# Kernel optimization log

Measured on AMD Instinct MI355X. Metric: run time of the kernel, lower is better.

Reference implementation:

```python
import jax, jax.numpy as jnp
import numpy as np

N_NODES = 100000
IN_DIM = 512
OUT_DIM = 16
N_EDGES = 3200000


def setup_inputs() -> dict:
    key = jax.random.key(0)
    k1, k2, k3, k4 = jax.random.split(key, 4)
    x = jax.random.normal(k1, (N_NODES, IN_DIM), dtype=jnp.float32)
    edge_index = jax.random.randint(k2, (2, N_EDGES), 0, N_NODES, dtype=jnp.int64)
    # GCNConv params (glorot weight, zero bias as in PyG)
    scale = jnp.sqrt(6.0 / (IN_DIM + OUT_DIM)).astype(jnp.float32)
    W = jax.random.uniform(k3, (IN_DIM, OUT_DIM), dtype=jnp.float32, minval=-scale, maxval=scale)
    b = jnp.zeros((OUT_DIM,), dtype=jnp.float32)
    return {"x": x, "edge_index": edge_index, "W": W, "b": b}


def reference(x, edge_index, W, b):
    n = x.shape[0]
    # GCNConv with normalize=True: add self-loops, symmetric deg normalization
    loops = jnp.arange(n, dtype=edge_index.dtype)
    row = jnp.concatenate([edge_index[0], loops])  # source nodes
    col = jnp.concatenate([edge_index[1], loops])  # target nodes

    h = x @ W  # [N, 16] dense linear transform

    deg = jax.ops.segment_sum(jnp.ones_like(col, dtype=h.dtype), col, num_segments=n)
    dinv = jnp.where(deg > 0, jax.lax.rsqrt(jnp.maximum(deg, 1.0)), 0.0)
    norm = dinv[row] * dinv[col]  # [E+N]

    # gather source features, scale, scatter-add into targets
    out = jax.ops.segment_sum(norm[:, None] * h[row], col, num_segments=n)
    return out + b
```

## Files before the change

kernel.cpp:

```cpp
#include <hip/hip_runtime.h>
#include <hip/hip_fp16.h>

#define IN_DIM 512
#define OUT_DIM 16
#define KC 32
#define TILE_ROWS 256

#define BSHIFT 8
#define BNODES 256
#define MAXBUCK 512
#define BCOUNT_CHUNK 4096
#define BIN_CHUNK 4096

__global__ __launch_bounds__(256) void gemm_wave(const float* __restrict__ x,
                                                 const float* __restrict__ W,
                                                 const int* __restrict__ hist,
                                                 __half* __restrict__ hp, int n) {
    __shared__ float xs[4 * 64 * (KC + 1)];
    const int tid = threadIdx.x;
    const int lane = tid & 63;
    const int wid = __builtin_amdgcn_readfirstlane(tid >> 6);
    const int rbase = blockIdx.x * 256 + wid * 64;
    if (rbase >= n) return;
    const int myrow = rbase + lane;

    float* xw = xs + wid * (64 * (KC + 1));
    const int srow = lane >> 3;
    const int scol = (lane & 7) << 2;

    float4 stA[8], stB[8];

#define LOADC(buf, c)                                                          \
    {                                                                          \
        _Pragma("unroll")                                                      \
        for (int i = 0; i < 8; ++i) {                                          \
            const int rr = rbase + 8 * i + srow;                               \
            if (rr < n)                                                        \
                buf[i] = *(const float4*)(x + (size_t)rr * IN_DIM + (c) * KC + scol); \
            else                                                               \
                buf[i] = make_float4(0.f, 0.f, 0.f, 0.f);                      \
        }                                                                      \
    }

#define STOREC(buf)                                                            \
    {                                                                          \
        _Pragma("unroll")                                                      \
        for (int i = 0; i < 8; ++i) {                                          \
            float* d = xw + (8 * i + srow) * (KC + 1) + scol;                  \
            d[0] = buf[i].x; d[1] = buf[i].y; d[2] = buf[i].z; d[3] = buf[i].w; \
        }                                                                      \
    }

#define COMPUTEC(c)                                                            \
    {                                                                          \
        const float* xrow = xw + lane * (KC + 1);                              \
        const float* Wb = W + (size_t)(c) * KC * OUT_DIM;                      \
        _Pragma("unroll 4")                                                    \
        for (int k = 0; k < KC; ++k) {                                         \
            const float xv = xrow[k];                                          \
            const float* wr = Wb + k * OUT_DIM;                                \
            const float4 w0 = *(const float4*)(wr + 0);                        \
            const float4 w1 = *(const float4*)(wr + 4);                        \
            const float4 w2 = *(const float4*)(wr + 8);                        \
            const float4 w3 = *(const float4*)(wr + 12);                       \
            acc[0]  += xv * w0.x; acc[1]  += xv * w0.y; acc[2]  += xv * w0.z; acc[3]  += xv * w0.w; \
            acc[4]  += xv * w1.x; acc[5]  += xv * w1.y; acc[6]  += xv * w1.z; acc[7]  += xv * w1.w; \
            acc[8]  += xv * w2.x; acc[9]  += xv * w2.y; acc[10] += xv * w2.z; acc[11] += xv * w2.w; \
            acc[12] += xv * w3.x; acc[13] += xv * w3.y; acc[14] += xv * w3.z; acc[15] += xv * w3.w; \
        }                                                                      \
    }

    float acc[OUT_DIM];
#pragma unroll
    for (int j = 0; j < OUT_DIM; ++j) acc[j] = 0.f;

    LOADC(stA, 0);
    for (int cc = 0; cc < 8; ++cc) {
        const int c0 = 2 * cc, c1 = 2 * cc + 1;
        STOREC(stA);
        LOADC(stB, c1);
        COMPUTEC(c0);
        STOREC(stB);
        if (c1 + 1 < 16) LOADC(stA, c1 + 1);
        COMPUTEC(c1);
    }

    if (myrow < n) {
        const float s = rsqrtf((float)(hist[myrow] + 1));
        __half2* op = (__half2*)(hp + (size_t)myrow * OUT_DIM);
#pragma unroll
        for (int j = 0; j < 8; ++j)
            op[j] = __floats2half2_rn(s * acc[2 * j], s * acc[2 * j + 1]);
    }
#undef LOADC
#undef STOREC
#undef COMPUTEC
}

__global__ __launch_bounds__(256) void gemm_xw(const float* __restrict__ x,
                                               const float* __restrict__ W,
                                               const int* __restrict__ hist,
                                               __half* __restrict__ hp, int n) {
    __shared__ float xs[TILE_ROWS * (KC + 1)];
    const int tid = threadIdx.x;
    const int rbase = blockIdx.x * TILE_ROWS;
    const int myrow = rbase + tid;

    float acc[OUT_DIM];
#pragma unroll
    for (int j = 0; j < OUT_DIM; ++j) acc[j] = 0.f;

    for (int kc = 0; kc < IN_DIM; kc += KC) {
        __syncthreads();
#pragma unroll
        for (int i = 0; i < 8; ++i) {
            const int v = tid + 256 * i;
            const int r = v >> 3;
            const int c = (v & 7) << 2;
            if (rbase + r < n) {
                const float4 f = *(const float4*)(x + (size_t)(rbase + r) * IN_DIM + kc + c);
                float* d = xs + r * (KC + 1) + c;
                d[0] = f.x; d[1] = f.y; d[2] = f.z; d[3] = f.w;
            }
        }
        __syncthreads();

        const float* xrow = xs + tid * (KC + 1);
#pragma unroll 4
        for (int k = 0; k < KC; ++k) {
            const float xv = xrow[k];
            const float* wr = W + (size_t)(kc + k) * OUT_DIM;
            const float4 w0 = *(const float4*)(wr + 0);
            const float4 w1 = *(const float4*)(wr + 4);
            const float4 w2 = *(const float4*)(wr + 8);
            const float4 w3 = *(const float4*)(wr + 12);
            acc[0]  += xv * w0.x; acc[1]  += xv * w0.y; acc[2]  += xv * w0.z; acc[3]  += xv * w0.w;
            acc[4]  += xv * w1.x; acc[5]  += xv * w1.y; acc[6]  += xv * w1.z; acc[7]  += xv * w1.w;
            acc[8]  += xv * w2.x; acc[9]  += xv * w2.y; acc[10] += xv * w2.z; acc[11] += xv * w2.w;
            acc[12] += xv * w3.x; acc[13] += xv * w3.y; acc[14] += xv * w3.z; acc[15] += xv * w3.w;
        }
    }

    if (myrow < n) {
        const float s = rsqrtf((float)(hist[myrow] + 1));
        __half2* op = (__half2*)(hp + (size_t)myrow * OUT_DIM);
#pragma unroll
        for (int j = 0; j < 8; ++j)
            op[j] = __floats2half2_rn(s * acc[2 * j], s * acc[2 * j + 1]);
    }
}

__device__ inline void scan512_excl(const int* src, int* dst, int lane) {
    int c[8], pre[8];
    int tot = 0;
#pragma unroll
    for (int k = 0; k < 8; ++k) { c[k] = src[lane * 8 + k]; pre[k] = tot; tot += c[k]; }
    int incl = tot;
#pragma unroll
    for (int d = 1; d < 64; d <<= 1) {
        const int u = __shfl_up(incl, d);
        if (lane >= d) incl += u;
    }
    const int excl = incl - tot;
#pragma unroll
    for (int k = 0; k < 8; ++k) dst[lane * 8 + k] = excl + pre[k];
}

__device__ inline void scan256_excl(const int* src, int* dst, int lane) {
    int c[4], pre[4];
    int tot = 0;
#pragma unroll
    for (int k = 0; k < 4; ++k) { c[k] = src[lane * 4 + k]; pre[k] = tot; tot += c[k]; }
    int incl = tot;
#pragma unroll
    for (int d = 1; d < 64; d <<= 1) {
        const int u = __shfl_up(incl, d);
        if (lane >= d) incl += u;
    }
    const int excl = incl - tot;
#pragma unroll
    for (int k = 0; k < 4; ++k) dst[lane * 4 + k] = excl + pre[k];
}

__global__ __launch_bounds__(256) void bcount(const int* __restrict__ dst,
                                              int* __restrict__ bcnt, int E, int nbuck) {
    __shared__ int lhist[MAXBUCK];
    const int tid = threadIdx.x;
    for (int i = tid; i < MAXBUCK; i += 256) lhist[i] = 0;
    __syncthreads();

    const int base = blockIdx.x * BCOUNT_CHUNK + tid * 16;
#pragma unroll
    for (int g = 0; g < 4; ++g) {
        const int e = base + g * 4;
        if (e + 3 < E) {
            const int4 d = *(const int4*)(dst + e);
            atomicAdd(&lhist[d.x >> BSHIFT], 1);
            atomicAdd(&lhist[d.y >> BSHIFT], 1);
            atomicAdd(&lhist[d.z >> BSHIFT], 1);
            atomicAdd(&lhist[d.w >> BSHIFT], 1);
        } else {
            for (int u = 0; u < 4; ++u)
                if (e + u < E) atomicAdd(&lhist[dst[e + u] >> BSHIFT], 1);
        }
    }
    __syncthreads();
    for (int i = tid; i < nbuck; i += 256)
        if (lhist[i] > 0) atomicAdd(&bcnt[i], lhist[i]);
}

__global__ __launch_bounds__(512) void bucket_scan(const int* __restrict__ bcnt,
                                                   int* __restrict__ bbase,
                                                   int* __restrict__ bcur, int nbuck) {
    __shared__ int sm[MAXBUCK];
    const int t = threadIdx.x;
    sm[t] = (t < nbuck) ? bcnt[t] : 0;
    __syncthreads();
    if (t < 64) scan512_excl(sm, sm, t);
    __syncthreads();
    bbase[t] = sm[t];
    bcur[t] = sm[t];
}

__global__ __launch_bounds__(256) void bin_edges(const int* __restrict__ ei,
                                                 int* __restrict__ bcur,
                                                 int* __restrict__ bins,
                                                 int E, int nbuck) {
    __shared__ int lhist[MAXBUCK];
    __shared__ int lbase[MAXBUCK];
    __shared__ int gbase[MAXBUCK];
    __shared__ int stage[BIN_CHUNK];
    __shared__ short sbkt[BIN_CHUNK];

    const int tid = threadIdx.x;
    const int e0 = blockIdx.x * BIN_CHUNK;
    const int cnt = min(BIN_CHUNK, E - e0);

    for (int i = tid; i < MAXBUCK; i += 256) lhist[i] = 0;
    __syncthreads();

    int myb[16], myr[16], myp[16];
    const int base = e0 + tid * 16;
#pragma unroll
    for (int g = 0; g < 4; ++g) {
        const int e = base + g * 4;
        int ss[4], dd[4];
        if ((E & 3) == 0 && e + 3 < E) {
            const int4 s4 = *(const int4*)(ei + e);
            const int4 d4 = *(const int4*)(ei + (size_t)E + e);
            ss[0] = s4.x; ss[1] = s4.y; ss[2] = s4.z; ss[3] = s4.w;
            dd[0] = d4.x; dd[1] = d4.y; dd[2] = d4.z; dd[3] = d4.w;
        } else {
#pragma unroll
            for (int u = 0; u < 4; ++u) {
                const int idx = e + u;
                ss[u] = (idx < E) ? ei[idx] : -1;
                dd[u] = (idx < E) ? ei[(size_t)E + idx] : 0;
            }
        }
#pragma unroll
        for (int u = 0; u < 4; ++u) {
            const int j = g * 4 + u;
            if (ss[u] >= 0) {
                const int bk = dd[u] >> BSHIFT;
                myb[j] = bk;
                myp[j] = (ss[u] << BSHIFT) | (dd[u] & (BNODES - 1));
                myr[j] = atomicAdd(&lhist[bk], 1);
            } else {
                myb[j] = -1; myr[j] = 0; myp[j] = 0;
            }
        }
    }
    __syncthreads();

    if (tid < 64) scan512_excl(lhist, lbase, tid);
    for (int i = tid; i < nbuck; i += 256)
        if (lhist[i] > 0) gbase[i] = atomicAdd(&bcur[i], lhist[i]);
    __syncthreads();

#pragma unroll
    for (int j = 0; j < 16; ++j) {
        if (myb[j] >= 0) {
            const int p = lbase[myb[j]] + myr[j];
            stage[p] = myp[j];
            sbkt[p] = (short)myb[j];
        }
    }
    __syncthreads();

    for (int i = tid; i < cnt; i += 256) {
        const int bk = sbkt[i];
        bins[gbase[bk] + (i - lbase[bk])] = stage[i];
    }
}

__global__ __launch_bounds__(1024) void bucket_sort(const int* __restrict__ bins,
                                                    const int* __restrict__ bbase,
                                                    const int* __restrict__ bcur,
                                                    int* __restrict__ csr,
                                                    int* __restrict__ hist,
                                                    int* __restrict__ off, int n) {
    __shared__ int nhist[BNODES];
    __shared__ int nbase[BNODES];
    __shared__ int ncur[BNODES];
    const int tid = threadIdx.x;
    const int b = blockIdx.x;
    const int s = bbase[b];
    const int e = bcur[b];

    if (tid < BNODES) nhist[tid] = 0;
    __syncthreads();
    for (int i = s + tid; i < e; i += 1024)
        atomicAdd(&nhist[bins[i] & (BNODES - 1)], 1);
    __syncthreads();
    if (tid < 64) scan256_excl(nhist, nbase, tid);
    __syncthreads();

    if (tid < BNODES) {
        const int node = (b << BSHIFT) + tid;
        if (node < n) {
            hist[node] = nhist[tid];
            off[node] = s + nbase[tid];
        }
        ncur[tid] = nbase[tid];
    }
    __syncthreads();

    for (int i = s + tid; i < e; i += 1024) {
        const int p = bins[i];
        const int r = atomicAdd(&ncur[p & (BNODES - 1)], 1);
        csr[s + r] = p >> BSHIFT;
    }
}

__global__ __launch_bounds__(256) void gather_out(const int* __restrict__ csr,
                                                  const int* __restrict__ off,
                                                  const int* __restrict__ hist,
                                                  const __half* __restrict__ hp,
                                                  const float* __restrict__ b,
                                                  float* __restrict__ out, int n) {
    const long long gid = (long long)blockIdx.x * 256 + threadIdx.x;
    const int d = (int)(gid >> 3);
    const int j2 = (int)(gid & 7);
    if (d >= n) return;

    const int base = off[d];
    const int deg = hist[d];
    const __half2* hpt = (const __half2*)hp;

    const __half2 sv = hpt[(size_t)d * 8 + j2];
    float ax = __low2float(sv), ay = __high2float(sv);

    int k = 0;
    for (; k + 4 <= deg; k += 4) {
        const int s0 = csr[base + k + 0];
        const int s1 = csr[base + k + 1];
        const int s2 = csr[base + k + 2];
        const int s3 = csr[base + k + 3];
        const __half2 v0 = hpt[(size_t)s0 * 8 + j2];
        const __half2 v1 = hpt[(size_t)s1 * 8 + j2];
        const __half2 v2 = hpt[(size_t)s2 * 8 + j2];
        const __half2 v3 = hpt[(size_t)s3 * 8 + j2];
        ax += __low2float(v0) + __low2float(v1) + __low2float(v2) + __low2float(v3);
        ay += __high2float(v0) + __high2float(v1) + __high2float(v2) + __high2float(v3);
    }
    for (; k < deg; ++k) {
        const __half2 v = hpt[(size_t)csr[base + k] * 8 + j2];
        ax += __low2float(v);
        ay += __high2float(v);
    }

    const float di = rsqrtf((float)(deg + 1));
    float2 o;
    o.x = di * ax + b[2 * j2];
    o.y = di * ay + b[2 * j2 + 1];
    ((float2*)out)[(size_t)d * 8 + j2] = o;
}

__global__ void hist_dst(const int* __restrict__ dst, int* __restrict__ hist, int E) {
    const int t = blockIdx.x * 256 + threadIdx.x;
    const int e0 = t * 4;
    if ((E & 3) == 0 && e0 + 3 < E) {
        const int4 d = *(const int4*)(dst + e0);
        atomicAdd(&hist[d.x], 1);
        atomicAdd(&hist[d.y], 1);
        atomicAdd(&hist[d.z], 1);
        atomicAdd(&hist[d.w], 1);
    } else {
        for (int e = e0; e < E && e < e0 + 4; ++e) atomicAdd(&hist[dst[e]], 1);
    }
}

__global__ __launch_bounds__(256) void scatter_f16(const int* __restrict__ ei,
                                                   const __half* __restrict__ hp,
                                                   __half2* __restrict__ acc, int E) {
    const long long gid = (long long)blockIdx.x * 256 + threadIdx.x;
    const int g = (int)(gid >> 3);
    const int j2 = (int)(gid & 7);
    const int e0 = g * 4;
    if (e0 >= E) return;

    int src[4], dst[4];
#pragma unroll
    for (int u = 0; u < 4; ++u) {
        const int e = e0 + u;
        src[u] = (e < E) ? ei[e] : -1;
        dst[u] = (e < E) ? ei[(size_t)E + e] : -1;
    }
    __half2 v[4];
#pragma unroll
    for (int u = 0; u < 4; ++u)
        if (src[u] >= 0) v[u] = ((const __half2*)(hp + (size_t)src[u] * OUT_DIM))[j2];
#pragma unroll
    for (int u = 0; u < 4; ++u)
        if (dst[u] >= 0) unsafeAtomicAdd(&acc[(size_t)dst[u] * 8 + j2], v[u]);
}

__global__ void finalize(const __half* __restrict__ acc, const __half* __restrict__ hp,
                         const int* __restrict__ hist, const float* __restrict__ b,
                         float* __restrict__ out, int n) {
    const int gid = blockIdx.x * 256 + threadIdx.x;
    if (gid >= n * OUT_DIM) return;
    const int i = gid >> 4;
    const int j = gid & 15;
    const float di = rsqrtf((float)(hist[i] + 1));
    out[gid] = di * (__half2float(acc[gid]) + __half2float(hp[gid])) + b[j];
}


extern "C" void kernel_launch(void* const* d_in, const int* in_sizes, int n_in,
                              void* d_out, int out_size, void* d_ws, size_t ws_size,
                              hipStream_t stream) {
    const float* x  = (const float*)d_in[0];
    const int*   ei = (const int*)d_in[1];
    const float* W  = (const float*)d_in[2];
    const float* b  = (const float*)d_in[3];
    float* out = (float*)d_out;

    const int n = in_sizes[0] / IN_DIM;
    const int E = in_sizes[1] / 2;
    const int nbuck = (n + BNODES - 1) >> BSHIFT;

    __half* hp    = (__half*)d_ws;
    int*    hist  = (int*)(hp + (size_t)n * OUT_DIM);
    int*    off   = hist + n;
    int*    bbase = off + n;
    int*    bcur  = bbase + MAXBUCK;
    int*    bcnt  = bcur + MAXBUCK;
    int*    bins  = bcnt + MAXBUCK;
    int*    csr   = bins + (size_t)E;

    const size_t need = (size_t)n * OUT_DIM * sizeof(__half)
                      + ((size_t)2 * n + 3 * MAXBUCK) * sizeof(int)
                      + 2 * (size_t)E * sizeof(int);

    if (ws_size >= need && nbuck <= MAXBUCK && n < (1 << 23)) {
        hipMemsetAsync(bcnt, 0, MAXBUCK * sizeof(int), stream);

        bcount<<<(E + BCOUNT_CHUNK - 1) / BCOUNT_CHUNK, 256, 0, stream>>>(ei + E, bcnt, E, nbuck);
        bucket_scan<<<1, 512, 0, stream>>>(bcnt, bbase, bcur, nbuck);
        bin_edges<<<(E + BIN_CHUNK - 1) / BIN_CHUNK, 256, 0, stream>>>(ei, bcur, bins, E, nbuck);
        bucket_sort<<<nbuck, 1024, 0, stream>>>(bins, bbase, bcur, csr, hist, off, n);
        gemm_wave<<<(n + 255) / 256, 256, 0, stream>>>(x, W, hist, hp, n);
        gather_out<<<(int)(((size_t)n * 8 + 255) / 256), 256, 0, stream>>>(csr, off, hist, hp, b, out, n);
    } else {
        __half* acc = (__half*)(hist + n);
        hipMemsetAsync(hist, 0, (size_t)n * sizeof(int), stream);
        hipMemsetAsync(acc, 0, (size_t)n * OUT_DIM * sizeof(__half), stream);

        hist_dst<<<(E + 1023) / 1024, 256, 0, stream>>>(ei + E, hist, E);
        gemm_xw<<<(n + TILE_ROWS - 1) / TILE_ROWS, 256, 0, stream>>>(x, W, hist, hp, n);
        const long long st = ((long long)(E + 3) / 4) * 8;
        scatter_f16<<<(int)((st + 255) / 256), 256, 0, stream>>>(ei, hp, (__half2*)acc, E);
        finalize<<<(n * OUT_DIM + 255) / 256, 256, 0, stream>>>(acc, hp, hist, b, out, n);
    }
}
```

Baseline: 428.3 us.

## Split GEMM K dimension across waves with shared-memory partial-sum reduction

After: 401.7 us. 1.07x faster.

```diff
diff --git a/kernel.cpp b/kernel.cpp
--- a/kernel.cpp
+++ b/kernel.cpp
@@ -12,21 +12,21 @@
 #define BCOUNT_CHUNK 4096
 #define BIN_CHUNK 4096
 
-__global__ __launch_bounds__(256) void gemm_wave(const float* __restrict__ x,
-                                                 const float* __restrict__ W,
-                                                 const int* __restrict__ hist,
-                                                 __half* __restrict__ hp, int n) {
+__global__ __launch_bounds__(256) void gemm_hybrid(const float* __restrict__ x,
+                                                   const float* __restrict__ W,
+                                                   const int* __restrict__ hist,
+                                                   __half* __restrict__ hp, int n) {
     __shared__ float xs[4 * 64 * (KC + 1)];
     const int tid = threadIdx.x;
     const int lane = tid & 63;
-    const int wid = __builtin_amdgcn_readfirstlane(tid >> 6);
-    const int rbase = blockIdx.x * 256 + wid * 64;
-    if (rbase >= n) return;
+    const int w = __builtin_amdgcn_readfirstlane(tid >> 6);
+    const int rbase = blockIdx.x * 64;
     const int myrow = rbase + lane;
 
-    float* xw = xs + wid * (64 * (KC + 1));
+    float* xw = xs + w * (64 * (KC + 1));
     const int srow = lane >> 3;
     const int scol = (lane & 7) << 2;
+    const int kbase = w * 128;
 
     float4 stA[8], stB[8];
 
@@ -36,7 +36,7 @@
         for (int i = 0; i < 8; ++i) {                                          \
             const int rr = rbase + 8 * i + srow;                               \
             if (rr < n)                                                        \
-                buf[i] = *(const float4*)(x + (size_t)rr * IN_DIM + (c) * KC + scol); \
+                buf[i] = *(const float4*)(x + (size_t)rr * IN_DIM + kbase + (c) * KC + scol); \
             else                                                               \
                 buf[i] = make_float4(0.f, 0.f, 0.f, 0.f);                      \
         }                                                                      \
@@ -54,7 +54,7 @@
 #define COMPUTEC(c)                                                            \
     {                                                                          \
         const float* xrow = xw + lane * (KC + 1);                              \
-        const float* Wb = W + (size_t)(c) * KC * OUT_DIM;                      \
+        const float* Wb = W + (size_t)(kbase + (c) * KC) * OUT_DIM;            \
         _Pragma("unroll 4")                                                    \
         for (int k = 0; k < KC; ++k) {                                         \
             const float xv = xrow[k];                                          \
@@ -75,22 +75,30 @@
     for (int j = 0; j < OUT_DIM; ++j) acc[j] = 0.f;
 
     LOADC(stA, 0);
-    for (int cc = 0; cc < 8; ++cc) {
-        const int c0 = 2 * cc, c1 = 2 * cc + 1;
-        STOREC(stA);
-        LOADC(stB, c1);
-        COMPUTEC(c0);
-        STOREC(stB);
-        if (c1 + 1 < 16) LOADC(stA, c1 + 1);
-        COMPUTEC(c1);
-    }
-
-    if (myrow < n) {
+    STOREC(stA); LOADC(stB, 1); COMPUTEC(0);
+    STOREC(stB); LOADC(stA, 2); COMPUTEC(1);
+    STOREC(stA); LOADC(stB, 3); COMPUTEC(2);
+    STOREC(stB);                COMPUTEC(3);
+
+    __syncthreads();
+    if (w > 0) {
+        float* d = xs + (w - 1) * (64 * 17) + lane * 17;
+#pragma unroll
+        for (int j = 0; j < OUT_DIM; ++j) d[j] = acc[j];
+    }
+    __syncthreads();
+    if (tid < 64 && myrow < n) {
+        const float* p0 = xs + 0 * (64 * 17) + tid * 17;
+        const float* p1 = xs + 1 * (64 * 17) + tid * 17;
+        const float* p2 = xs + 2 * (64 * 17) + tid * 17;
         const float s = rsqrtf((float)(hist[myrow] + 1));
         __half2* op = (__half2*)(hp + (size_t)myrow * OUT_DIM);
 #pragma unroll
-        for (int j = 0; j < 8; ++j)
-            op[j] = __floats2half2_rn(s * acc[2 * j], s * acc[2 * j + 1]);
+        for (int j = 0; j < 8; ++j) {
+            const float lo = acc[2 * j]     + p0[2 * j]     + p1[2 * j]     + p2[2 * j];
+            const float hi = acc[2 * j + 1] + p0[2 * j + 1] + p1[2 * j + 1] + p2[2 * j + 1];
+            op[j] = __floats2half2_rn(s * lo, s * hi);
+        }
     }
 #undef LOADC
 #undef STOREC
@@ -461,7 +469,7 @@
         bucket_scan<<<1, 512, 0, stream>>>(bcnt, bbase, bcur, nbuck);
         bin_edges<<<(E + BIN_CHUNK - 1) / BIN_CHUNK, 256, 0, stream>>>(ei, bcur, bins, E, nbuck);
         bucket_sort<<<nbuck, 1024, 0, stream>>>(bins, bbase, bcur, csr, hist, off, n);
-        gemm_wave<<<(n + 255) / 256, 256, 0, stream>>>(x, W, hist, hp, n);
+        gemm_hybrid<<<(n + 63) / 64, 256, 0, stream>>>(x, W, hist, hp, n);
         gather_out<<<(int)(((size_t)n * 8 + 255) / 256), 256, 0, stream>>>(csr, off, hist, hp, b, out, n);
     } else {
         __half* acc = (__half*)(hist + n);
```
